# Kernel tuning notes

Hardware: AMD Instinct MI355X
Metric: run time of the kernel (lower is better)

## Reference

```python
import jax, jax.numpy as jnp
import numpy as np

BH, L, D = 64, 1024, 128

def setup_inputs() -> dict:
    key = jax.random.key(0)
    k1, k2, k3 = jax.random.split(key, 3)
    q = jax.random.normal(k1, (BH, L, D), dtype=jnp.float32)
    k = jax.random.normal(k2, (BH, L, D), dtype=jnp.float32)
    v = jax.random.normal(k3, (BH, L, D), dtype=jnp.float32)
    # causal multiplicative mask, broadcast to all batch*head slices
    attn_mask = jnp.broadcast_to(jnp.tril(jnp.ones((L, L), dtype=jnp.float32)), (BH, L, L))
    return {"q": q, "k": k, "v": v, "attn_mask": attn_mask}

def reference(q, k, v, attn_mask):
    # NOTE: original module computes self.temper = dim_dec**0.5 but never uses it,
    # so scores are UNscaled. Dropout is identity at eval.
    attn = jnp.einsum('bqd,bkd->bqk', q, k)          # [BH, L, L]
    attn = attn * attn_mask                           # multiplicative mask on logits
    attn = jnp.exp(attn - jnp.max(attn))              # GLOBAL max subtraction (not per-row)
    attn = attn * attn_mask                           # mask again after exp
    attn = attn / (jnp.sum(attn, axis=2, keepdims=True) + 1e-15)
    return jnp.einsum('bqk,bkd->bqd', attn, v)        # [BH, L, D]
```

## Files before the change

### kernel.cpp

```cpp
#include <hip/hip_runtime.h>
#include <hip/hip_bf16.h>

#define BHN 64
#define LSEQ 1024
#define DIM 128
#define BM 64
#define BN 64
#define NQB (LSEQ / BM)

typedef _Float16 f16x4 __attribute__((ext_vector_type(4)));
typedef _Float16 f16x8 __attribute__((ext_vector_type(8)));
typedef float f32x4 __attribute__((ext_vector_type(4)));

__global__ __launch_bounds__(256, 4) void attn_pass1(
    const float* __restrict__ Q, const float* __restrict__ K,
    const float* __restrict__ V, float* __restrict__ Out,
    float* __restrict__ mrow, float* __restrict__ rrow, float* __restrict__ gmax)
{
    __shared__ _Float16 Kf[BN][136];
    __shared__ _Float16 Vt[DIM][72];

    const int tid  = threadIdx.x;
    const int lane = tid & 63;
    const int wave = tid >> 6;
    const int g    = lane >> 4;
    const int ln   = lane & 15;
    const int L    = blockIdx.x;
    const int qb   = (NQB - 1) - (L >> 6);
    const int bh   = L & 63;
    const int qrow0 = qb * BM + wave * 16;

    const float* qp = Q + (size_t)bh * LSEQ * DIM;
    const float* kp = K + (size_t)bh * LSEQ * DIM;
    const float* vp = V + (size_t)bh * LSEQ * DIM;

    const int vd = tid & 127;
    const int vh = tid >> 7;

    f16x8 qf[4];
    {
        const float* qrow = qp + (size_t)(qrow0 + ln) * DIM;
        #pragma unroll
        for (int kc = 0; kc < 4; ++kc) {
            const int d0 = kc * 32 + g * 8;
            float4 f0 = *(const float4*)(qrow + d0);
            float4 f1 = *(const float4*)(qrow + d0 + 4);
            f16x8 h;
            h[0] = (_Float16)f0.x; h[1] = (_Float16)f0.y;
            h[2] = (_Float16)f0.z; h[3] = (_Float16)f0.w;
            h[4] = (_Float16)f1.x; h[5] = (_Float16)f1.y;
            h[6] = (_Float16)f1.z; h[7] = (_Float16)f1.w;
            qf[kc] = h;
        }
    }

    float m_st = -1e30f, r_st = 0.f;
    f32x4 o_acc[8];
    #pragma unroll
    for (int d = 0; d < 8; ++d) { f32x4 z = {0.f,0.f,0.f,0.f}; o_acc[d] = z; }

    const int nt = qb + 1;
    for (int t = 0; t < nt; ++t) {
        const int kv0 = t * BN;
        __syncthreads();

        #pragma unroll
        for (int i = 0; i < 8; ++i) {
            const int f4  = i * 256 + tid;
            const int row = f4 >> 5;
            const int c   = (f4 & 31) * 4;
            float4 kk = *(const float4*)(kp + (size_t)(kv0 + row) * DIM + c);
            f16x4 h4;
            h4[0] = (_Float16)kk.x; h4[1] = (_Float16)kk.y;
            h4[2] = (_Float16)kk.z; h4[3] = (_Float16)kk.w;
            *(f16x4*)&Kf[row][c] = h4;
        }
        #pragma unroll
        for (int nb = 0; nb < 4; ++nb) {
            const int n0 = vh * 32 + nb * 8;
            float tmp[8];
            #pragma unroll
            for (int i = 0; i < 8; ++i)
                tmp[i] = vp[(size_t)(kv0 + n0 + i) * DIM + vd];
            f16x8 w;
            #pragma unroll
            for (int i = 0; i < 8; ++i) w[i] = (_Float16)tmp[i];
            *(f16x8*)&Vt[vd][n0] = w;
        }
        __syncthreads();

        f32x4 sacc[4];
        #pragma unroll
        for (int ns = 0; ns < 4; ++ns) { f32x4 z = {0.f,0.f,0.f,0.f}; sacc[ns] = z; }
        #pragma unroll
        for (int ns = 0; ns < 4; ++ns) {
            const int n = ns * 16 + ln;
            #pragma unroll
            for (int kc = 0; kc < 4; ++kc) {
                f16x8 kh_ = *(const f16x8*)&Kf[n][kc * 32 + g * 8];
                sacc[ns] = __builtin_amdgcn_mfma_f32_16x16x32_f16(kh_, qf[kc], sacc[ns], 0, 0, 0);
            }
        }

        if (t == qb) {
            const int qm = qrow0 + ln - kv0 - 4 * g;
            #pragma unroll
            for (int ns = 0; ns < 4; ++ns)
                #pragma unroll
                for (int j = 0; j < 4; ++j)
                    if (16 * ns + j > qm) sacc[ns][j] = -1e30f;
        }

        float tm = -1e30f;
        #pragma unroll
        for (int ns = 0; ns < 4; ++ns)
            #pragma unroll
            for (int j = 0; j < 4; ++j) tm = fmaxf(tm, sacc[ns][j]);
        tm = fmaxf(tm, __shfl_xor(tm, 16));
        tm = fmaxf(tm, __shfl_xor(tm, 32));
        const float mn = fmaxf(m_st, tm);
        const float sc = __expf(m_st - mn);
        float pr[4][4];
        float ts = 0.f;
        #pragma unroll
        for (int ns = 0; ns < 4; ++ns)
            #pragma unroll
            for (int j = 0; j < 4; ++j) {
                const float pv = __expf(sacc[ns][j] - mn);
                pr[ns][j] = pv;
                ts += pv;
            }
        ts += __shfl_xor(ts, 16);
        ts += __shfl_xor(ts, 32);
        r_st = r_st * sc + ts;
        m_st = mn;

        float scr[4];
        #pragma unroll
        for (int r = 0; r < 4; ++r) scr[r] = __shfl(sc, 4 * g + r);
        #pragma unroll
        for (int d = 0; d < 8; ++d) {
            o_acc[d][0] *= scr[0]; o_acc[d][1] *= scr[1];
            o_acc[d][2] *= scr[2]; o_acc[d][3] *= scr[3];
        }

        f16x8 pa0, pa1;
        #pragma unroll
        for (int j = 0; j < 4; ++j) {
            pa0[j]     = (_Float16)pr[0][j];
            pa0[4 + j] = (_Float16)pr[1][j];
            pa1[j]     = (_Float16)pr[2][j];
            pa1[4 + j] = (_Float16)pr[3][j];
        }
        #pragma unroll
        for (int ds = 0; ds < 8; ++ds) {
            const int dc = ds * 16 + ln;
            f16x4 v0 = *(const f16x4*)&Vt[dc][4 * g];
            f16x4 v1 = *(const f16x4*)&Vt[dc][16 + 4 * g];
            f16x8 bv0;
            #pragma unroll
            for (int j = 0; j < 4; ++j) { bv0[j] = v0[j]; bv0[4 + j] = v1[j]; }
            o_acc[ds] = __builtin_amdgcn_mfma_f32_16x16x32_f16(pa0, bv0, o_acc[ds], 0, 0, 0);
            f16x4 v2 = *(const f16x4*)&Vt[dc][32 + 4 * g];
            f16x4 v3 = *(const f16x4*)&Vt[dc][48 + 4 * g];
            f16x8 bv1;
            #pragma unroll
            for (int j = 0; j < 4; ++j) { bv1[j] = v2[j]; bv1[4 + j] = v3[j]; }
            o_acc[ds] = __builtin_amdgcn_mfma_f32_16x16x32_f16(pa1, bv1, o_acc[ds], 0, 0, 0);
        }
    }

    #pragma unroll
    for (int ds = 0; ds < 8; ++ds) {
        const int dc = ds * 16 + ln;
        #pragma unroll
        for (int r = 0; r < 4; ++r) {
            const int qr = qrow0 + g * 4 + r;
            Out[((size_t)bh * LSEQ + qr) * DIM + dc] = o_acc[ds][r];
        }
    }
    if (lane < 16) {
        mrow[bh * LSEQ + qrow0 + lane] = m_st;
        rrow[bh * LSEQ + qrow0 + lane] = r_st;
    }
    float bm = m_st;
    #pragma unroll
    for (int off = 32; off >= 1; off >>= 1) bm = fmaxf(bm, __shfl_xor(bm, off));
    if (lane == 0) atomicMax((int*)gmax, __float_as_int(bm));
}

__global__ __launch_bounds__(256) void attn_epilogue(
    float* __restrict__ Out, const float* __restrict__ mrow,
    const float* __restrict__ rrow, const float* __restrict__ gmax)
{
    const int idx = blockIdx.x * 256 + threadIdx.x;
    const int row = idx >> 5;
    const float M = *gmax;
    float e = M - mrow[row] - 34.538776394910684f;
    e = fminf(e, 85.f);
    const float denom = rrow[row] + __expf(e);
    const float inv = 1.0f / denom;
    float4 o = ((float4*)Out)[idx];
    o.x *= inv; o.y *= inv; o.z *= inv; o.w *= inv;
    ((float4*)Out)[idx] = o;
}

extern "C" void kernel_launch(void* const* d_in, const int* in_sizes, int n_in,
                              void* d_out, int out_size, void* d_ws, size_t ws_size,
                              hipStream_t stream)
{
    const float* q = (const float*)d_in[0];
    const float* k = (const float*)d_in[1];
    const float* v = (const float*)d_in[2];
    float* out  = (float*)d_out;
    float* mrow = (float*)d_ws;
    float* rrow = mrow + BHN * LSEQ;
    float* gmax = rrow + BHN * LSEQ;

    hipMemsetAsync(gmax, 0, sizeof(float), stream);

    attn_pass1<<<dim3(BHN * NQB), 256, 0, stream>>>(q, k, v, out, mrow, rrow, gmax);

    const int n4 = BHN * LSEQ * DIM / 4;
    attn_epilogue<<<n4 / 256, 256, 0, stream>>>(out, mrow, rrow, gmax);
}
```

Measured before the change: 109.9 us.

## Pair causal q-blocks per workgroup and prefetch K/V tiles through registers

Each workgroup now handles two query blocks, p and NQB-1-p, so the causal work per block is balanced and the grid halves to 512 workgroups. K/V tiles for the next step are loaded into registers while the current tile is being computed, with a double-buffered LDS layout, so global latency overlaps MFMA work. The prefetch chain carries over from the first query block to the second. Launch bounds drop to 2 waves per SIMD, and doubled LDS plus the extra prefetch registers may reduce occupancy.

```diff
diff --git a/kernel.cpp b/kernel.cpp
--- a/kernel.cpp
+++ b/kernel.cpp
@@ -12,23 +12,21 @@
 typedef _Float16 f16x8 __attribute__((ext_vector_type(8)));
 typedef float f32x4 __attribute__((ext_vector_type(4)));
 
-__global__ __launch_bounds__(256, 4) void attn_pass1(
+__global__ __launch_bounds__(256, 2) void attn_pass1(
     const float* __restrict__ Q, const float* __restrict__ K,
     const float* __restrict__ V, float* __restrict__ Out,
     float* __restrict__ mrow, float* __restrict__ rrow, float* __restrict__ gmax)
 {
-    __shared__ _Float16 Kf[BN][136];
-    __shared__ _Float16 Vt[DIM][72];
+    __shared__ _Float16 Kf[2][BN][136];
+    __shared__ _Float16 Vt[2][DIM][72];
 
     const int tid  = threadIdx.x;
+    const int wave = tid >> 6;
     const int lane = tid & 63;
-    const int wave = tid >> 6;
     const int g    = lane >> 4;
     const int ln   = lane & 15;
-    const int L    = blockIdx.x;
-    const int qb   = (NQB - 1) - (L >> 6);
-    const int bh   = L & 63;
-    const int qrow0 = qb * BM + wave * 16;
+    const int bh   = blockIdx.x;
+    const int p    = blockIdx.y;
 
     const float* qp = Q + (size_t)bh * LSEQ * DIM;
     const float* kp = K + (size_t)bh * LSEQ * DIM;
@@ -37,156 +35,191 @@
     const int vd = tid & 127;
     const int vh = tid >> 7;
 
-    f16x8 qf[4];
-    {
-        const float* qrow = qp + (size_t)(qrow0 + ln) * DIM;
-        #pragma unroll
-        for (int kc = 0; kc < 4; ++kc) {
-            const int d0 = kc * 32 + g * 8;
-            float4 f0 = *(const float4*)(qrow + d0);
-            float4 f1 = *(const float4*)(qrow + d0 + 4);
-            f16x8 h;
-            h[0] = (_Float16)f0.x; h[1] = (_Float16)f0.y;
-            h[2] = (_Float16)f0.z; h[3] = (_Float16)f0.w;
-            h[4] = (_Float16)f1.x; h[5] = (_Float16)f1.y;
-            h[6] = (_Float16)f1.z; h[7] = (_Float16)f1.w;
-            qf[kc] = h;
-        }
-    }
-
-    float m_st = -1e30f, r_st = 0.f;
-    f32x4 o_acc[8];
-    #pragma unroll
-    for (int d = 0; d < 8; ++d) { f32x4 z = {0.f,0.f,0.f,0.f}; o_acc[d] = z; }
-
-    const int nt = qb + 1;
-    for (int t = 0; t < nt; ++t) {
-        const int kv0 = t * BN;
-        __syncthreads();
-
+    float4 kreg[8];
+    float  vreg[4][8];
+
+    auto issue = [&](int kv0) {
         #pragma unroll
         for (int i = 0; i < 8; ++i) {
             const int f4  = i * 256 + tid;
             const int row = f4 >> 5;
             const int c   = (f4 & 31) * 4;
-            float4 kk = *(const float4*)(kp + (size_t)(kv0 + row) * DIM + c);
-            f16x4 h4;
-            h4[0] = (_Float16)kk.x; h4[1] = (_Float16)kk.y;
-            h4[2] = (_Float16)kk.z; h4[3] = (_Float16)kk.w;
-            *(f16x4*)&Kf[row][c] = h4;
-        }
-        #pragma unroll
-        for (int nb = 0; nb < 4; ++nb) {
-            const int n0 = vh * 32 + nb * 8;
-            float tmp[8];
+            kreg[i] = *(const float4*)(kp + (size_t)(kv0 + row) * DIM + c);
+        }
+        #pragma unroll
+        for (int nb = 0; nb < 4; ++nb)
             #pragma unroll
             for (int i = 0; i < 8; ++i)
-                tmp[i] = vp[(size_t)(kv0 + n0 + i) * DIM + vd];
-            f16x8 w;
-            #pragma unroll
-            for (int i = 0; i < 8; ++i) w[i] = (_Float16)tmp[i];
-            *(f16x8*)&Vt[vd][n0] = w;
-        }
-        __syncthreads();
-
-        f32x4 sacc[4];
-        #pragma unroll
-        for (int ns = 0; ns < 4; ++ns) { f32x4 z = {0.f,0.f,0.f,0.f}; sacc[ns] = z; }
-        #pragma unroll
-        for (int ns = 0; ns < 4; ++ns) {
-            const int n = ns * 16 + ln;
+                vreg[nb][i] = vp[(size_t)(kv0 + vh * 32 + nb * 8 + i) * DIM + vd];
+    };
+
+    int cur = 0;
+    issue(0);
+
+    for (int s = 0; s < 2; ++s) {
+        const int qb    = s ? (NQB - 1 - p) : p;
+        const int qrow0 = qb * BM + wave * 16;
+
+        f16x8 qf[4];
+        {
+            const float* qrow = qp + (size_t)(qrow0 + ln) * DIM;
             #pragma unroll
             for (int kc = 0; kc < 4; ++kc) {
-                f16x8 kh_ = *(const f16x8*)&Kf[n][kc * 32 + g * 8];
-                sacc[ns] = __builtin_amdgcn_mfma_f32_16x16x32_f16(kh_, qf[kc], sacc[ns], 0, 0, 0);
-            }
-        }
-
-        if (t == qb) {
-            const int qm = qrow0 + ln - kv0 - 4 * g;
+                const int d0 = kc * 32 + g * 8;
+                float4 f0 = *(const float4*)(qrow + d0);
+                float4 f1 = *(const float4*)(qrow + d0 + 4);
+                f16x8 h;
+                h[0] = (_Float16)f0.x; h[1] = (_Float16)f0.y;
+                h[2] = (_Float16)f0.z; h[3] = (_Float16)f0.w;
+                h[4] = (_Float16)f1.x; h[5] = (_Float16)f1.y;
+                h[6] = (_Float16)f1.z; h[7] = (_Float16)f1.w;
+                qf[kc] = h;
+            }
+        }
+
+        float m_st = -1e30f, r_st = 0.f;
+        f32x4 o_acc[8];
+        #pragma unroll
+        for (int d = 0; d < 8; ++d) { f32x4 z = {0.f,0.f,0.f,0.f}; o_acc[d] = z; }
+
+        const int nt = qb + 1;
+        for (int t = 0; t < nt; ++t) {
+            const int kv0 = t * BN;
+
+            f16x4 khf[8];
+            #pragma unroll
+            for (int i = 0; i < 8; ++i) {
+                f16x4 h4;
+                h4[0] = (_Float16)kreg[i].x; h4[1] = (_Float16)kreg[i].y;
+                h4[2] = (_Float16)kreg[i].z; h4[3] = (_Float16)kreg[i].w;
+                khf[i] = h4;
+            }
+            f16x8 vbf[4];
+            #pragma unroll
+            for (int nb = 0; nb < 4; ++nb) {
+                f16x8 w;
+                #pragma unroll
+                for (int i = 0; i < 8; ++i) w[i] = (_Float16)vreg[nb][i];
+                vbf[nb] = w;
+            }
+
+            __syncthreads();
+            #pragma unroll
+            for (int i = 0; i < 8; ++i) {
+                const int f4  = i * 256 + tid;
+                const int row = f4 >> 5;
+                const int c   = (f4 & 31) * 4;
+                *(f16x4*)&Kf[cur][row][c] = khf[i];
+            }
+            #pragma unroll
+            for (int nb = 0; nb < 4; ++nb)
+                *(f16x8*)&Vt[cur][vd][vh * 32 + nb * 8] = vbf[nb];
+            __syncthreads();
+
+            const int nxt = (t + 1 < nt) ? (t + 1) * BN : (s == 0 ? 0 : -1);
+            if (nxt >= 0) issue(nxt);
+
+            f32x4 sacc[4];
+            #pragma unroll
+            for (int ns = 0; ns < 4; ++ns) { f32x4 z = {0.f,0.f,0.f,0.f}; sacc[ns] = z; }
+            #pragma unroll
+            for (int ns = 0; ns < 4; ++ns) {
+                const int n = ns * 16 + ln;
+                #pragma unroll
+                for (int kc = 0; kc < 4; ++kc) {
+                    f16x8 kh_ = *(const f16x8*)&Kf[cur][n][kc * 32 + g * 8];
+                    sacc[ns] = __builtin_amdgcn_mfma_f32_16x16x32_f16(kh_, qf[kc], sacc[ns], 0, 0, 0);
+                }
+            }
+
+            if (t == qb) {
+                const int qm = qrow0 + ln - kv0 - 4 * g;
+                #pragma unroll
+                for (int ns = 0; ns < 4; ++ns)
+                    #pragma unroll
+                    for (int j = 0; j < 4; ++j)
+                        if (16 * ns + j > qm) sacc[ns][j] = -1e30f;
+            }
+
+            float tm = -1e30f;
             #pragma unroll
             for (int ns = 0; ns < 4; ++ns)
                 #pragma unroll
-                for (int j = 0; j < 4; ++j)
-                    if (16 * ns + j > qm) sacc[ns][j] = -1e30f;
-        }
-
-        float tm = -1e30f;
-        #pragma unroll
-        for (int ns = 0; ns < 4; ++ns)
-            #pragma unroll
-            for (int j = 0; j < 4; ++j) tm = fmaxf(tm, sacc[ns][j]);
-        tm = fmaxf(tm, __shfl_xor(tm, 16));
-        tm = fmaxf(tm, __shfl_xor(tm, 32));
-        const float mn = fmaxf(m_st, tm);
-        const float sc = __expf(m_st - mn);
-        float pr[4][4];
-        float ts = 0.f;
-        #pragma unroll
-        for (int ns = 0; ns < 4; ++ns)
+                for (int j = 0; j < 4; ++j) tm = fmaxf(tm, sacc[ns][j]);
+            tm = fmaxf(tm, __shfl_xor(tm, 16));
+            tm = fmaxf(tm, __shfl_xor(tm, 32));
+            const float mn = fmaxf(m_st, tm);
+            const float sc = __expf(m_st - mn);
+            float pr[4][4];
+            float ts = 0.f;
+            #pragma unroll
+            for (int ns = 0; ns < 4; ++ns)
+                #pragma unroll
+                for (int j = 0; j < 4; ++j) {
+                    const float pv = __expf(sacc[ns][j] - mn);
+                    pr[ns][j] = pv;
+                    ts += pv;
+                }
+            ts += __shfl_xor(ts, 16);
+            ts += __shfl_xor(ts, 32);
+            r_st = r_st * sc + ts;
+            m_st = mn;
+
+            float scr[4];
+            #pragma unroll
+            for (int r = 0; r < 4; ++r) scr[r] = __shfl(sc, 4 * g + r);
+            #pragma unroll
+            for (int d = 0; d < 8; ++d) {
+                o_acc[d][0] *= scr[0]; o_acc[d][1] *= scr[1];
+                o_acc[d][2] *= scr[2]; o_acc[d][3] *= scr[3];
+            }
+
+            f16x8 pa0, pa1;
             #pragma unroll
             for (int j = 0; j < 4; ++j) {
-                const float pv = __expf(sacc[ns][j] - mn);
-                pr[ns][j] = pv;
-                ts += pv;
-            }
-        ts += __shfl_xor(ts, 16);
-        ts += __shfl_xor(ts, 32);
-        r_st = r_st * sc + ts;
-        m_st = mn;
-
-        float scr[4];
-        #pragma unroll
-        for (int r = 0; r < 4; ++r) scr[r] = __shfl(sc, 4 * g + r);
-        #pragma unroll
-        for (int d = 0; d < 8; ++d) {
-            o_acc[d][0] *= scr[0]; o_acc[d][1] *= scr[1];
-            o_acc[d][2] *= scr[2]; o_acc[d][3] *= scr[3];
-        }
-
-        f16x8 pa0, pa1;
-        #pragma unroll
-        for (int j = 0; j < 4; ++j) {
-            pa0[j]     = (_Float16)pr[0][j];
-            pa0[4 + j] = (_Float16)pr[1][j];
-            pa1[j]     = (_Float16)pr[2][j];
-            pa1[4 + j] = (_Float16)pr[3][j];
-        }
+                pa0[j]     = (_Float16)pr[0][j];
+                pa0[4 + j] = (_Float16)pr[1][j];
+                pa1[j]     = (_Float16)pr[2][j];
+                pa1[4 + j] = (_Float16)pr[3][j];
+            }
+            #pragma unroll
+            for (int ds = 0; ds < 8; ++ds) {
+                const int dc = ds * 16 + ln;
+                f16x4 v0 = *(const f16x4*)&Vt[cur][dc][4 * g];
+                f16x4 v1 = *(const f16x4*)&Vt[cur][dc][16 + 4 * g];
+                f16x8 bv0;
+                #pragma unroll
+                for (int j = 0; j < 4; ++j) { bv0[j] = v0[j]; bv0[4 + j] = v1[j]; }
+                o_acc[ds] = __builtin_amdgcn_mfma_f32_16x16x32_f16(pa0, bv0, o_acc[ds], 0, 0, 0);
+                f16x4 v2 = *(const f16x4*)&Vt[cur][dc][32 + 4 * g];
+                f16x4 v3 = *(const f16x4*)&Vt[cur][dc][48 + 4 * g];
+                f16x8 bv1;
+                #pragma unroll
+                for (int j = 0; j < 4; ++j) { bv1[j] = v2[j]; bv1[4 + j] = v3[j]; }
+                o_acc[ds] = __builtin_amdgcn_mfma_f32_16x16x32_f16(pa1, bv1, o_acc[ds], 0, 0, 0);
+            }
+
+            cur ^= 1;
+        }
+
         #pragma unroll
         for (int ds = 0; ds < 8; ++ds) {
             const int dc = ds * 16 + ln;
-            f16x4 v0 = *(const f16x4*)&Vt[dc][4 * g];
-            f16x4 v1 = *(const f16x4*)&Vt[dc][16 + 4 * g];
-            f16x8 bv0;
-            #pragma unroll
-            for (int j = 0; j < 4; ++j) { bv0[j] = v0[j]; bv0[4 + j] = v1[j]; }
-            o_acc[ds] = __builtin_amdgcn_mfma_f32_16x16x32_f16(pa0, bv0, o_acc[ds], 0, 0, 0);
-            f16x4 v2 = *(const f16x4*)&Vt[dc][32 + 4 * g];
-            f16x4 v3 = *(const f16x4*)&Vt[dc][48 + 4 * g];
-            f16x8 bv1;
-            #pragma unroll
-            for (int j = 0; j < 4; ++j) { bv1[j] = v2[j]; bv1[4 + j] = v3[j]; }
-            o_acc[ds] = __builtin_amdgcn_mfma_f32_16x16x32_f16(pa1, bv1, o_acc[ds], 0, 0, 0);
-        }
+            #pragma unroll
+            for (int r = 0; r < 4; ++r) {
+                const int qr = qrow0 + g * 4 + r;
+                Out[((size_t)bh * LSEQ + qr) * DIM + dc] = o_acc[ds][r];
+            }
+        }
+        if (lane < 16) {
+            mrow[bh * LSEQ + qrow0 + lane] = m_st;
+            rrow[bh * LSEQ + qrow0 + lane] = r_st;
+        }
+        float bm = m_st;
+        #pragma unroll
+        for (int off = 32; off >= 1; off >>= 1) bm = fmaxf(bm, __shfl_xor(bm, off));
+        if (lane == 0) atomicMax((int*)gmax, __float_as_int(bm));
     }
-
-    #pragma unroll
-    for (int ds = 0; ds < 8; ++ds) {
-        const int dc = ds * 16 + ln;
-        #pragma unroll
-        for (int r = 0; r < 4; ++r) {
-            const int qr = qrow0 + g * 4 + r;
-            Out[((size_t)bh * LSEQ + qr) * DIM + dc] = o_acc[ds][r];
-        }
-    }
-    if (lane < 16) {
-        mrow[bh * LSEQ + qrow0 + lane] = m_st;
-        rrow[bh * LSEQ + qrow0 + lane] = r_st;
-    }
-    float bm = m_st;
-    #pragma unroll
-    for (int off = 32; off >= 1; off >>= 1) bm = fmaxf(bm, __shfl_xor(bm, off));
-    if (lane == 0) atomicMax((int*)gmax, __float_as_int(bm));
 }
 
 __global__ __launch_bounds__(256) void attn_epilogue(
@@ -219,7 +252,8 @@
 
     hipMemsetAsync(gmax, 0, sizeof(float), stream);
 
-    attn_pass1<<<dim3(BHN * NQB), 256, 0, stream>>>(q, k, v, out, mrow, rrow, gmax);
+    dim3 grid(BHN, NQB / 2);
+    attn_pass1<<<grid, 256, 0, stream>>>(q, k, v, out, mrow, rrow, gmax);
 
     const int n4 = BHN * LSEQ * DIM / 4;
     attn_epilogue<<<n4 / 256, 256, 0, stream>>>(out, mrow, rrow, gmax);
```

New measurement: 96.07 us. 1.14x faster.
